# Kernel optimization log

Measured on AMD Instinct MI355X. Metric: run time of the kernel, lower is better.

The kernel has to match this reference:

```python
import jax, jax.numpy as jnp
import numpy as np

C_WEIGHT = 0.005  # 'c' hyperparameter

def _psi(v):
    return jnp.sign(v) * jnp.log1p(jnp.abs(v))

def setup_inputs() -> dict:
    key = jax.random.key(0)
    ks = jax.random.split(key, 16)
    B, P, C = 64, 128, 72
    s = lambda fan_in: 1.0 / np.sqrt(fan_in)
    return {
        'x': jax.random.normal(ks[0], (B, P, 4), dtype=jnp.float32),
        'h': jax.random.normal(ks[1], (B, P, C), dtype=jnp.float32),
        'We1': jax.random.normal(ks[2], (2 * C + 2, 72), dtype=jnp.float32) * s(2 * C + 2),
        'be1': jnp.zeros((72,), dtype=jnp.float32),
        'We2': jax.random.normal(ks[3], (72, 72), dtype=jnp.float32) * s(72),
        'be2': jnp.zeros((72,), dtype=jnp.float32),
        'Wm': jax.random.normal(ks[4], (72, 1), dtype=jnp.float32) * s(72),
        'bm': jnp.zeros((1,), dtype=jnp.float32),
        'Wh1': jax.random.normal(ks[5], (C + 72, 72), dtype=jnp.float32) * s(C + 72),
        'bh1': jnp.zeros((72,), dtype=jnp.float32),
        'Wh2': jax.random.normal(ks[6], (72, 72), dtype=jnp.float32) * s(72),
        'bh2': jnp.zeros((72,), dtype=jnp.float32),
        'Wx': jax.random.normal(ks[7], (72, 1), dtype=jnp.float32) * s(72),
    }

def reference(x, h, We1, be1, We2, be2, Wm, bm, Wh1, bh1, Wh2, bh2, Wx):
    B, P, _ = x.shape
    # pairwise Minkowski invariants: take(...,0)*2 - sum == t^2 - |vec|^2
    x1 = x[:, :, None, :]  # (B,P,1,4)
    x2 = x[:, None, :, :]  # (B,1,P,4)
    d2 = jnp.square(x1 - x2)                      # (B,P,P,4)
    norms = 2.0 * d2[..., 0] - d2.sum(axis=-1)    # (B,P,P)
    z = x1 * x2
    prods = 2.0 * z[..., 0] - z.sum(axis=-1)      # (B,P,P)
    norms = _psi(norms)[..., None]                # use_psi=True
    prods = _psi(prods)[..., None]
    H = h.shape[-1]
    h1 = jnp.broadcast_to(h[:, :, None, :], (B, P, P, H))
    h2 = jnp.broadcast_to(h[:, None, :, :], (B, P, P, H))
    feat = jnp.concatenate([h1, h2, norms, prods], axis=-1)  # (B,P,P,2H+2)
    # phi_e: two Dense+ReLU
    m = jax.nn.relu(feat @ We1 + be1)
    m = jax.nn.relu(m @ We2 + be2)                # (B,P,P,72)
    # phi_m: Dense(1) + sigmoid
    w = jax.nn.sigmoid(m @ Wm + bm)               # (B,P,P,1)
    wm = jnp.sum(w * m, axis=2)                   # (B,P,72)
    # phi_h: Dense+ReLU, Dense; residual add
    g = jax.nn.relu(jnp.concatenate([h, wm], axis=-1) @ Wh1 + bh1)
    dh = g @ Wh2 + bh2
    h_out = h + dh
    # phi_x: Dense(1, no bias); x update
    phi_x = m @ Wx                                # (B,P,P,1)
    x_out = x + C_WEIGHT * jnp.mean(phi_x * x[:, None, :, :], axis=2)
    return (h_out, x_out)
```

## Files before the change

### kernel.cpp

```cpp
#include <hip/hip_runtime.h>
#include <hip/hip_bf16.h>
#include <math.h>

#define B_ 64
#define P_ 128
#define C_ 72
#define PADC 80
#define BCS 88
#define IT 8

typedef __attribute__((ext_vector_type(8))) _Float16 half8v;
typedef __attribute__((ext_vector_type(4))) float f32x4;
typedef __attribute__((ext_vector_type(2))) float f32x2;
typedef __attribute__((ext_vector_type(4))) unsigned int u32x4;

#define FRAG_WE2  0
#define FRAG_WE1A (15 * 64)
#define FRAG_WE1B (30 * 64)
#define FRAG_WH1  (45 * 64)
#define FRAG_WH2  (70 * 64)
#define NFRAG 85

__device__ __forceinline__ float psi_f(float v) {
    float a = fabsf(v);
    return copysignf(__logf(1.0f + a), v);
}
template <int CTRL>
__device__ __forceinline__ float dpp_add(float v) {
    int s = __builtin_amdgcn_update_dpp(0, __builtin_bit_cast(int, v), CTRL, 0xF, 0xF, true);
    return v + __builtin_bit_cast(float, s);
}
__device__ __forceinline__ float red16(float v) {
    v = dpp_add<0xB1>(v);
    v = dpp_add<0x4E>(v);
    v = dpp_add<0x141>(v);
    v = dpp_add<0x140>(v);
    return v;
}
__device__ __forceinline__ half8v cvt8(const float* p) {
    f32x4 a = *(const f32x4*)p;
    f32x4 b = *(const f32x4*)(p + 4);
    half8v r = {(_Float16)a[0], (_Float16)a[1], (_Float16)a[2], (_Float16)a[3],
                (_Float16)b[0], (_Float16)b[1], (_Float16)b[2], (_Float16)b[3]};
    return r;
}

__global__ __launch_bounds__(64) void setup_kernel(
    const float* __restrict__ We1, const float* __restrict__ be1,
    const float* __restrict__ We2, const float* __restrict__ be2,
    const float* __restrict__ Wh1, const float* __restrict__ bh1,
    const float* __restrict__ Wh2, const float* __restrict__ bh2,
    half8v* __restrict__ frags)
{
    const int bid = blockIdx.x;
    const int l = threadIdx.x;
    const int c16 = l & 15, g = l >> 4;

    const float* W;
    const float* bias;
    int kmax, rel;
    if (bid < 15)      { W = We2;            bias = be2;     kmax = 72;  rel = bid; }
    else if (bid < 30) { W = We1;            bias = nullptr; kmax = 72;  rel = bid - 15; }
    else if (bid < 45) { W = We1 + 72 * C_;  bias = be1;     kmax = 72;  rel = bid - 30; }
    else if (bid < 70) { W = Wh1;            bias = bh1;     kmax = 144; rel = bid - 45; }
    else               { W = Wh2;            bias = bh2;     kmax = 72;  rel = bid - 70; }
    const int kt = rel / 5, nt = rel - 5 * kt;
    const int n = nt * 16 + c16;

    half8v f = {};
    if (n < C_) {
        #pragma unroll
        for (int jj = 0; jj < 8; ++jj) {
            int k = kt * 32 + g * 8 + jj;
            float w = 0.f;
            if (k < kmax) w = W[k * C_ + n];
            else if (k == kmax && bias) w = bias[n];
            f[jj] = (_Float16)w;
        }
    }
    frags[bid * 64 + l] = f;
}

__global__ __launch_bounds__(64) void pre_kernel(
    const float* __restrict__ h, const half8v* __restrict__ frags,
    _Float16* __restrict__ Ah, _Float16* __restrict__ Bch)
{
    const int l = threadIdx.x, c16 = l & 15, g = l >> 4;
    const int m0 = blockIdx.x * 16;

    const float* hrow = h + (m0 + c16) * C_;
    half8v a0 = cvt8(hrow + g * 8);
    half8v a1 = cvt8(hrow + 32 + g * 8);
    half8v a2 = {};
    if (g == 0) a2 = cvt8(hrow + 64);
    else if (g == 1) a2[0] = (_Float16)1.0f;

    #pragma unroll 1
    for (int sel = 0; sel < 2; ++sel) {
        const half8v* F = frags + (sel ? FRAG_WE1B : FRAG_WE1A);
        f32x4 acc[5] = {};
        #pragma unroll
        for (int kt = 0; kt < 3; ++kt) {
            half8v a = (kt == 0) ? a0 : (kt == 1 ? a1 : a2);
            #pragma unroll
            for (int nt = 0; nt < 5; ++nt)
                acc[nt] = __builtin_amdgcn_mfma_f32_16x16x32_f16(a, F[(kt * 5 + nt) * 64 + l], acc[nt], 0, 0, 0);
        }
        _Float16* dst = sel ? Bch : Ah;
        #pragma unroll
        for (int nt = 0; nt < 5; ++nt) {
            int n = nt * 16 + c16;
            if (n < C_) {
                #pragma unroll
                for (int r = 0; r < 4; ++r)
                    dst[(m0 + 4 * g + r) * PADC + n] = (_Float16)acc[nt][r];
            }
        }
    }
}

__global__ __launch_bounds__(256, 2) void edge_kernel(
    const float* __restrict__ x, const _Float16* __restrict__ Ah,
    const _Float16* __restrict__ Bch, const float* __restrict__ We1,
    const half8v* __restrict__ frags,
    const float* __restrict__ Wm, const float* __restrict__ bm,
    const float* __restrict__ Wx,
    float* __restrict__ wm_out, float* __restrict__ xacc_out)
{
    __shared__ __align__(16) _Float16 A_s[IT][PADC];
    __shared__ __align__(16) _Float16 Bc_s[P_][BCS];
    __shared__ __align__(16) float xj_s[P_][4];
    __shared__ __align__(16) _Float16 w1_s[PADC], w2_s[PADC];

    const int b  = blockIdx.x >> 4;
    const int it = blockIdx.x & 15;
    const int t  = threadIdx.x;
    const int wv = t >> 6;
    const int l  = t & 63;
    const int c16 = l & 15;
    const int g   = l >> 4;

    {
        const unsigned int* Asrc = (const unsigned int*)(Ah + (b * P_ + it * IT) * PADC);
        for (int idx = t; idx < IT * PADC / 2; idx += 256)
            ((unsigned int*)A_s)[idx] = Asrc[idx];
        for (int cidx = t; cidx < P_ * 10; cidx += 256) {
            int r = cidx / 10, c = cidx - r * 10;
            *(u32x4*)&Bc_s[r][c * 8] = ((const u32x4*)(Bch + (b * P_ + r) * PADC))[c];
        }
        for (int idx = t; idx < P_ * 4; idx += 256)
            ((float*)xj_s)[idx] = x[b * P_ * 4 + idx];
        if (t < 160) {
            int hs = t >= 80;
            int c = t - hs * 80;
            float wv_ = (c < C_) ? We1[(144 + hs) * C_ + c] : 0.f;
            (hs ? w2_s : w1_s)[c] = (_Float16)wv_;
        }
    }
    __syncthreads();

    half8v Wf[3][5];
    #pragma unroll
    for (int kt = 0; kt < 3; ++kt)
        #pragma unroll
        for (int nt = 0; nt < 5; ++nt)
            Wf[kt][nt] = frags[FRAG_WE2 + (kt * 5 + nt) * 64 + l];

    f32x2 WmWx[5][4];
    #pragma unroll
    for (int nt = 0; nt < 5; ++nt)
        #pragma unroll
        for (int r = 0; r < 4; ++r) {
            int ch = nt * 16 + 4 * g + r;
            bool ok = ch < C_;
            WmWx[nt][r][0] = ok ? Wm[ch] : 0.f;
            WmWx[nt][r][1] = ok ? Wx[ch] : 0.f;
        }
    const float bm0 = bm[0];
    const f32x4 zero4 = {0.f, 0.f, 0.f, 0.f};

    #pragma unroll 1
    for (int ii = 0; ii < 2; ++ii) {
        const int iloc = wv * 2 + ii;
        const int i = it * IT + iloc;
        const int node_i = b * P_ + i;
        const f32x4 xi = *(const f32x4*)&xj_s[i][0];

        f32x4 wmacc[5] = {};
        f32x4 xacc = {0.f, 0.f, 0.f, 0.f};

        #pragma unroll 1
        for (int jt = 0; jt < 8; ++jt) {
            const int j = jt * 16 + c16;
            const f32x4 xjv = *(const f32x4*)&xj_s[j][0];
            float d0 = xi[0] - xjv[0], d1 = xi[1] - xjv[1];
            float d2 = xi[2] - xjv[2], d3 = xi[3] - xjv[3];
            float nn = d0 * d0 - d1 * d1 - d2 * d2 - d3 * d3;
            float pp = xi[0] * xjv[0] - xi[1] * xjv[1] - xi[2] * xjv[2] - xi[3] * xjv[3];
            _Float16 nh = (_Float16)psi_f(nn);
            _Float16 ph = (_Float16)psi_f(pp);
            half8v n8 = {nh, nh, nh, nh, nh, nh, nh, nh};
            half8v p8 = {ph, ph, ph, ph, ph, ph, ph, ph};
            half8v zero8 = {};

            auto chunk = [&](int k) -> half8v {
                half8v av = *(const half8v*)&A_s[iloc][k];
                half8v bv = *(const half8v*)&Bc_s[j][k];
                half8v w1 = *(const half8v*)&w1_s[k];
                half8v w2 = *(const half8v*)&w2_s[k];
                half8v v = av + bv;
                v = __builtin_elementwise_fma(w1, n8, v);
                v = __builtin_elementwise_fma(w2, p8, v);
                return __builtin_elementwise_max(v, zero8);
            };
            half8v af0 = chunk(g * 8);
            half8v af1 = chunk(32 + g * 8);
            half8v af2 = {};
            if (g == 0) af2 = chunk(64);
            else if (g == 1) af2[0] = (_Float16)1.0f;

            f32x4 acc[5] = {};
            #pragma unroll
            for (int nt = 0; nt < 5; ++nt)
                acc[nt] = __builtin_amdgcn_mfma_f32_16x16x32_f16(Wf[0][nt], af0, acc[nt], 0, 0, 0);
            #pragma unroll
            for (int nt = 0; nt < 5; ++nt)
                acc[nt] = __builtin_amdgcn_mfma_f32_16x16x32_f16(Wf[1][nt], af1, acc[nt], 0, 0, 0);
            #pragma unroll
            for (int nt = 0; nt < 5; ++nt)
                acc[nt] = __builtin_amdgcn_mfma_f32_16x16x32_f16(Wf[2][nt], af2, acc[nt], 0, 0, 0);

            f32x2 wdpd = {0.f, 0.f};
            #pragma unroll
            for (int nt = 0; nt < 5; ++nt) {
                f32x4 m2q = __builtin_elementwise_max(acc[nt], zero4);
                acc[nt] = m2q;
                #pragma unroll
                for (int r = 0; r < 4; ++r) {
                    f32x2 vv = {m2q[r], m2q[r]};
                    wdpd = __builtin_elementwise_fma(vv, WmWx[nt][r], wdpd);
                }
            }
            {
                f32x2 s;
                s[0] = __shfl_xor(wdpd[0], 16, 64);
                s[1] = __shfl_xor(wdpd[1], 16, 64);
                wdpd += s;
                s[0] = __shfl_xor(wdpd[0], 32, 64);
                s[1] = __shfl_xor(wdpd[1], 32, 64);
                wdpd += s;
            }
            float w_ = __builtin_amdgcn_rcpf(1.f + __expf(-(wdpd[0] + bm0)));
            f32x4 w4 = {w_, w_, w_, w_};
            #pragma unroll
            for (int nt = 0; nt < 5; ++nt)
                wmacc[nt] = __builtin_elementwise_fma(w4, acc[nt], wmacc[nt]);
            f32x4 pd4 = {wdpd[1], wdpd[1], wdpd[1], wdpd[1]};
            xacc = __builtin_elementwise_fma(pd4, xjv, xacc);
        }

        #pragma unroll
        for (int nt = 0; nt < 5; ++nt)
            #pragma unroll
            for (int r = 0; r < 4; ++r)
                wmacc[nt][r] = red16(wmacc[nt][r]);
        #pragma unroll
        for (int q = 0; q < 4; ++q) xacc[q] = red16(xacc[q]);

        if (c16 == 0) {
            #pragma unroll
            for (int nt = 0; nt < 5; ++nt)
                #pragma unroll
                for (int r = 0; r < 4; ++r) {
                    int ch = nt * 16 + 4 * g + r;
                    if (ch < C_) wm_out[node_i * C_ + ch] = wmacc[nt][r];
                }
        }
        if (l == 0)
            *(f32x4*)&xacc_out[node_i * 4] = xacc;
    }
}

__global__ __launch_bounds__(64) void node_kernel(
    const float* __restrict__ x, const float* __restrict__ h,
    const half8v* __restrict__ frags,
    const float* __restrict__ wm, const float* __restrict__ xacc,
    float* __restrict__ hout, float* __restrict__ xout)
{
    __shared__ _Float16 g_s[16][BCS];
    const int l = threadIdx.x, c16 = l & 15, g = l >> 4;
    const int m0 = blockIdx.x * 16;

    const float* hrow  = h  + (m0 + c16) * C_;
    const float* wmrow = wm + (m0 + c16) * C_;

    half8v a[5];
    #pragma unroll
    for (int kt = 0; kt < 5; ++kt) {
        int k = kt * 32 + g * 8;
        half8v v = {};
        if (k < C_) v = cvt8(hrow + k);
        else if (k < 144) v = cvt8(wmrow + (k - C_));
        else if (k == 144) v[0] = (_Float16)1.0f;
        a[kt] = v;
    }
    f32x4 acc1[5] = {};
    #pragma unroll
    for (int kt = 0; kt < 5; ++kt)
        #pragma unroll
        for (int nt = 0; nt < 5; ++nt)
            acc1[nt] = __builtin_amdgcn_mfma_f32_16x16x32_f16(
                a[kt], frags[FRAG_WH1 + (kt * 5 + nt) * 64 + l], acc1[nt], 0, 0, 0);

    #pragma unroll
    for (int nt = 0; nt < 5; ++nt) {
        int n = nt * 16 + c16;
        #pragma unroll
        for (int r = 0; r < 4; ++r)
            g_s[4 * g + r][n] = (_Float16)fmaxf(acc1[nt][r], 0.f);
    }
    half8v b0 = *(const half8v*)&g_s[c16][g * 8];
    half8v b1 = *(const half8v*)&g_s[c16][32 + g * 8];
    half8v b2 = {};
    if (g == 0) b2 = *(const half8v*)&g_s[c16][64];
    else if (g == 1) b2[0] = (_Float16)1.0f;

    f32x4 acc2[5] = {};
    #pragma unroll
    for (int kt = 0; kt < 3; ++kt) {
        half8v aa = (kt == 0) ? b0 : (kt == 1 ? b1 : b2);
        #pragma unroll
        for (int nt = 0; nt < 5; ++nt)
            acc2[nt] = __builtin_amdgcn_mfma_f32_16x16x32_f16(
                aa, frags[FRAG_WH2 + (kt * 5 + nt) * 64 + l], acc2[nt], 0, 0, 0);
    }
    #pragma unroll
    for (int nt = 0; nt < 5; ++nt) {
        int n = nt * 16 + c16;
        if (n < C_) {
            #pragma unroll
            for (int r = 0; r < 4; ++r) {
                int row = m0 + 4 * g + r;
                hout[row * C_ + n] = h[row * C_ + n] + acc2[nt][r];
            }
        }
    }
    {
        int row = m0 + (l >> 2), d = l & 3;
        xout[row * 4 + d] = x[row * 4 + d] + 0.005f * (xacc[row * 4 + d] * (1.0f / 128.f));
    }
}

extern "C" void kernel_launch(void* const* d_in, const int* in_sizes, int n_in,
                              void* d_out, int out_size, void* d_ws, size_t ws_size,
                              hipStream_t stream) {
    const float* x   = (const float*)d_in[0];
    const float* h   = (const float*)d_in[1];
    const float* We1 = (const float*)d_in[2];
    const float* be1 = (const float*)d_in[3];
    const float* We2 = (const float*)d_in[4];
    const float* be2 = (const float*)d_in[5];
    const float* Wm  = (const float*)d_in[6];
    const float* bm  = (const float*)d_in[7];
    const float* Wh1 = (const float*)d_in[8];
    const float* bh1 = (const float*)d_in[9];
    const float* Wh2 = (const float*)d_in[10];
    const float* bh2 = (const float*)d_in[11];
    const float* Wx  = (const float*)d_in[12];

    const int NNODE = B_ * P_;
    _Float16* Ah  = (_Float16*)d_ws;
    _Float16* Bch = Ah + NNODE * PADC;
    float* wm   = (float*)(Bch + NNODE * PADC);
    float* xacc = wm + NNODE * C_;
    half8v* frags = (half8v*)(xacc + NNODE * 4);

    float* hout = (float*)d_out;
    float* xout = hout + NNODE * C_;

    setup_kernel<<<NFRAG, 64, 0, stream>>>(We1, be1, We2, be2, Wh1, bh1, Wh2, bh2, frags);
    pre_kernel<<<NNODE / 16, 64, 0, stream>>>(h, frags, Ah, Bch);
    edge_kernel<<<B_ * 16, 256, 0, stream>>>(x, Ah, Bch, We1, frags,
                                             Wm, bm, Wx, wm, xacc);
    node_kernel<<<NNODE / 16, 64, 0, stream>>>(x, h, frags, wm, xacc, hout, xout);
}
```

Baseline: 61.82 us.

## Split pre_kernel over two blocks and hoist per-row edge operands into registers

pre_kernel now launches twice as many blocks, each computing only one of the two We1 projections (A or Bc) instead of looping over both, which adds parallelism. In edge_kernel the We1 norm and product rows are loaded straight into registers rather than staged in shared memory, and the A_s row chunks are loaded once per i instead of once per j tile. This cuts LDS reads in the inner loop. Wm/Wx are stored as half pairs to save registers, at the cost of small precision loss, and the paired-vector reduction is split into scalar FMAs and shuffles.

```diff
diff --git a/kernel.cpp b/kernel.cpp
--- a/kernel.cpp
+++ b/kernel.cpp
@@ -10,6 +10,7 @@
 #define IT 8
 
 typedef __attribute__((ext_vector_type(8))) _Float16 half8v;
+typedef __attribute__((ext_vector_type(2))) _Float16 half2v;
 typedef __attribute__((ext_vector_type(4))) float f32x4;
 typedef __attribute__((ext_vector_type(2))) float f32x2;
 typedef __attribute__((ext_vector_type(4))) unsigned int u32x4;
@@ -86,7 +87,8 @@
     _Float16* __restrict__ Ah, _Float16* __restrict__ Bch)
 {
     const int l = threadIdx.x, c16 = l & 15, g = l >> 4;
-    const int m0 = blockIdx.x * 16;
+    const int sel = blockIdx.x & 1;
+    const int m0 = (blockIdx.x >> 1) * 16;
 
     const float* hrow = h + (m0 + c16) * C_;
     half8v a0 = cvt8(hrow + g * 8);
@@ -95,26 +97,23 @@
     if (g == 0) a2 = cvt8(hrow + 64);
     else if (g == 1) a2[0] = (_Float16)1.0f;
 
-    #pragma unroll 1
-    for (int sel = 0; sel < 2; ++sel) {
-        const half8v* F = frags + (sel ? FRAG_WE1B : FRAG_WE1A);
-        f32x4 acc[5] = {};
-        #pragma unroll
-        for (int kt = 0; kt < 3; ++kt) {
-            half8v a = (kt == 0) ? a0 : (kt == 1 ? a1 : a2);
-            #pragma unroll
-            for (int nt = 0; nt < 5; ++nt)
-                acc[nt] = __builtin_amdgcn_mfma_f32_16x16x32_f16(a, F[(kt * 5 + nt) * 64 + l], acc[nt], 0, 0, 0);
-        }
-        _Float16* dst = sel ? Bch : Ah;
-        #pragma unroll
-        for (int nt = 0; nt < 5; ++nt) {
-            int n = nt * 16 + c16;
-            if (n < C_) {
-                #pragma unroll
-                for (int r = 0; r < 4; ++r)
-                    dst[(m0 + 4 * g + r) * PADC + n] = (_Float16)acc[nt][r];
-            }
+    const half8v* F = frags + (sel ? FRAG_WE1B : FRAG_WE1A);
+    f32x4 acc[5] = {};
+    #pragma unroll
+    for (int kt = 0; kt < 3; ++kt) {
+        half8v a = (kt == 0) ? a0 : (kt == 1 ? a1 : a2);
+        #pragma unroll
+        for (int nt = 0; nt < 5; ++nt)
+            acc[nt] = __builtin_amdgcn_mfma_f32_16x16x32_f16(a, F[(kt * 5 + nt) * 64 + l], acc[nt], 0, 0, 0);
+    }
+    _Float16* dst = sel ? Bch : Ah;
+    #pragma unroll
+    for (int nt = 0; nt < 5; ++nt) {
+        int n = nt * 16 + c16;
+        if (n < C_) {
+            #pragma unroll
+            for (int r = 0; r < 4; ++r)
+                dst[(m0 + 4 * g + r) * PADC + n] = (_Float16)acc[nt][r];
         }
     }
 }
@@ -130,7 +129,6 @@
     __shared__ __align__(16) _Float16 A_s[IT][PADC];
     __shared__ __align__(16) _Float16 Bc_s[P_][BCS];
     __shared__ __align__(16) float xj_s[P_][4];
-    __shared__ __align__(16) _Float16 w1_s[PADC], w2_s[PADC];
 
     const int b  = blockIdx.x >> 4;
     const int it = blockIdx.x & 15;
@@ -150,14 +148,16 @@
         }
         for (int idx = t; idx < P_ * 4; idx += 256)
             ((float*)xj_s)[idx] = x[b * P_ * 4 + idx];
-        if (t < 160) {
-            int hs = t >= 80;
-            int c = t - hs * 80;
-            float wv_ = (c < C_) ? We1[(144 + hs) * C_ + c] : 0.f;
-            (hs ? w2_s : w1_s)[c] = (_Float16)wv_;
-        }
-    }
-    __syncthreads();
+    }
+
+    const float* w1g = We1 + 144 * C_;
+    const float* w2g = We1 + 145 * C_;
+    half8v w1a = cvt8(w1g + g * 8);
+    half8v w1b = cvt8(w1g + 32 + g * 8);
+    half8v w1c = cvt8(w1g + 64);
+    half8v w2a = cvt8(w2g + g * 8);
+    half8v w2b = cvt8(w2g + 32 + g * 8);
+    half8v w2c = cvt8(w2g + 64);
 
     half8v Wf[3][5];
     #pragma unroll
@@ -166,18 +166,20 @@
         for (int nt = 0; nt < 5; ++nt)
             Wf[kt][nt] = frags[FRAG_WE2 + (kt * 5 + nt) * 64 + l];
 
-    f32x2 WmWx[5][4];
+    half2v WmWx[5][4];
     #pragma unroll
     for (int nt = 0; nt < 5; ++nt)
         #pragma unroll
         for (int r = 0; r < 4; ++r) {
             int ch = nt * 16 + 4 * g + r;
             bool ok = ch < C_;
-            WmWx[nt][r][0] = ok ? Wm[ch] : 0.f;
-            WmWx[nt][r][1] = ok ? Wx[ch] : 0.f;
+            WmWx[nt][r][0] = (_Float16)(ok ? Wm[ch] : 0.f);
+            WmWx[nt][r][1] = (_Float16)(ok ? Wx[ch] : 0.f);
         }
     const float bm0 = bm[0];
     const f32x4 zero4 = {0.f, 0.f, 0.f, 0.f};
+
+    __syncthreads();
 
     #pragma unroll 1
     for (int ii = 0; ii < 2; ++ii) {
@@ -185,6 +187,10 @@
         const int i = it * IT + iloc;
         const int node_i = b * P_ + i;
         const f32x4 xi = *(const f32x4*)&xj_s[i][0];
+
+        half8v ava = *(const half8v*)&A_s[iloc][g * 8];
+        half8v avb = *(const half8v*)&A_s[iloc][32 + g * 8];
+        half8v avc = *(const half8v*)&A_s[iloc][64];
 
         f32x4 wmacc[5] = {};
         f32x4 xacc = {0.f, 0.f, 0.f, 0.f};
@@ -203,20 +209,16 @@
             half8v p8 = {ph, ph, ph, ph, ph, ph, ph, ph};
             half8v zero8 = {};
 
-            auto chunk = [&](int k) -> half8v {
-                half8v av = *(const half8v*)&A_s[iloc][k];
-                half8v bv = *(const half8v*)&Bc_s[j][k];
-                half8v w1 = *(const half8v*)&w1_s[k];
-                half8v w2 = *(const half8v*)&w2_s[k];
-                half8v v = av + bv;
+            auto mk = [&](half8v av, const _Float16* bp, half8v w1, half8v w2) -> half8v {
+                half8v v = av + *(const half8v*)bp;
                 v = __builtin_elementwise_fma(w1, n8, v);
                 v = __builtin_elementwise_fma(w2, p8, v);
                 return __builtin_elementwise_max(v, zero8);
             };
-            half8v af0 = chunk(g * 8);
-            half8v af1 = chunk(32 + g * 8);
+            half8v af0 = mk(ava, &Bc_s[j][g * 8],      w1a, w2a);
+            half8v af1 = mk(avb, &Bc_s[j][32 + g * 8], w1b, w2b);
             half8v af2 = {};
-            if (g == 0) af2 = chunk(64);
+            if (g == 0) af2 = mk(avc, &Bc_s[j][64], w1c, w2c);
             else if (g == 1) af2[0] = (_Float16)1.0f;
 
             f32x4 acc[5] = {};
@@ -230,32 +232,28 @@
             for (int nt = 0; nt < 5; ++nt)
                 acc[nt] = __builtin_amdgcn_mfma_f32_16x16x32_f16(Wf[2][nt], af2, acc[nt], 0, 0, 0);
 
-            f32x2 wdpd = {0.f, 0.f};
+            float wd = 0.f, pd = 0.f;
             #pragma unroll
             for (int nt = 0; nt < 5; ++nt) {
                 f32x4 m2q = __builtin_elementwise_max(acc[nt], zero4);
                 acc[nt] = m2q;
                 #pragma unroll
                 for (int r = 0; r < 4; ++r) {
-                    f32x2 vv = {m2q[r], m2q[r]};
-                    wdpd = __builtin_elementwise_fma(vv, WmWx[nt][r], wdpd);
+                    wd = fmaf(m2q[r], (float)WmWx[nt][r][0], wd);
+                    pd = fmaf(m2q[r], (float)WmWx[nt][r][1], pd);
                 }
             }
-            {
-                f32x2 s;
-                s[0] = __shfl_xor(wdpd[0], 16, 64);
-                s[1] = __shfl_xor(wdpd[1], 16, 64);
-                wdpd += s;
-                s[0] = __shfl_xor(wdpd[0], 32, 64);
-                s[1] = __shfl_xor(wdpd[1], 32, 64);
-                wdpd += s;
-            }
-            float w_ = __builtin_amdgcn_rcpf(1.f + __expf(-(wdpd[0] + bm0)));
+            wd += __shfl_xor(wd, 16, 64);
+            pd += __shfl_xor(pd, 16, 64);
+            wd += __shfl_xor(wd, 32, 64);
+            pd += __shfl_xor(pd, 32, 64);
+
+            float w_ = __builtin_amdgcn_rcpf(1.f + __expf(-(wd + bm0)));
             f32x4 w4 = {w_, w_, w_, w_};
             #pragma unroll
             for (int nt = 0; nt < 5; ++nt)
                 wmacc[nt] = __builtin_elementwise_fma(w4, acc[nt], wmacc[nt]);
-            f32x4 pd4 = {wdpd[1], wdpd[1], wdpd[1], wdpd[1]};
+            f32x4 pd4 = {pd, pd, pd, pd};
             xacc = __builtin_elementwise_fma(pd4, xjv, xacc);
         }
 
@@ -379,7 +377,7 @@
     float* xout = hout + NNODE * C_;
 
     setup_kernel<<<NFRAG, 64, 0, stream>>>(We1, be1, We2, be2, Wh1, bh1, Wh2, bh2, frags);
-    pre_kernel<<<NNODE / 16, 64, 0, stream>>>(h, frags, Ah, Bch);
+    pre_kernel<<<NNODE / 16 * 2, 64, 0, stream>>>(h, frags, Ah, Bch);
     edge_kernel<<<B_ * 16, 256, 0, stream>>>(x, Ah, Bch, We1, frags,
                                              Wm, bm, Wx, wm, xacc);
     node_kernel<<<NNODE / 16, 64, 0, stream>>>(x, h, frags, wm, xacc, hout, xout);
```

Measured after the change: 62.12 us. Within noise of the previous version (+0.5%).
